# Kernel tuning notes

Measured on AMD Instinct MI355X. Metric: run time of the kernel, lower is better.

Reference implementation:

```python
import jax, jax.numpy as jnp
import numpy as np

N, E, D, H = 50000, 300000, 256, 2
C = D // H  # per-head out_channels (PyG TransformerConv, concat=True)
LN_EPS = 1e-5


def setup_inputs() -> dict:
    key = jax.random.key(0)
    ks = jax.random.split(key, 10)
    s = 1.0 / np.sqrt(D).astype(np.float32)
    return {
        "x": jax.random.normal(ks[0], (N, D), jnp.float32),
        "edge_attr": jax.random.normal(ks[1], (E, D), jnp.float32),
        "edge_index": jax.random.randint(ks[2], (2, E), 0, N, dtype=jnp.int32),
        "Wq": jax.random.normal(ks[3], (D, D), jnp.float32) * s,
        "bq": jnp.zeros((D,), jnp.float32),
        "Wk": jax.random.normal(ks[4], (D, D), jnp.float32) * s,
        "bk": jnp.zeros((D,), jnp.float32),
        "Wv": jax.random.normal(ks[5], (D, D), jnp.float32) * s,
        "bv": jnp.zeros((D,), jnp.float32),
        "We": jax.random.normal(ks[6], (D, D), jnp.float32) * s,  # lin_edge, bias=False in PyG
        "Wskip": jax.random.normal(ks[7], (D, D), jnp.float32) * s,
        "bskip": jnp.zeros((D,), jnp.float32),
        "ln_gamma": jnp.ones((D,), jnp.float32),
        "ln_beta": jnp.zeros((D,), jnp.float32),
    }


def reference(x, edge_attr, edge_index, Wq, bq, Wk, bk, Wv, bv, We,
              Wskip, bskip, ln_gamma, ln_beta):
    src, dst = edge_index[0], edge_index[1]  # message flows src(j) -> dst(i)

    # node-level projections (dense GEMMs), reshaped to [*, H, C]
    q = (x @ Wq + bq).reshape(N, H, C)
    k = (x @ Wk + bk).reshape(N, H, C)
    v = (x @ Wv + bv).reshape(N, H, C)
    e = (edge_attr @ We).reshape(E, H, C)

    # per-edge gather; edge features added to both key and value (PyG TransformerConv)
    k_e = k[src] + e            # [E, H, C]
    v_e = v[src] + e            # [E, H, C]

    # attention logits per edge/head, scaled by sqrt(C)
    alpha = jnp.einsum('ehc,ehc->eh', q[dst], k_e) / np.sqrt(C).astype(np.float32)

    # segment softmax over incoming edges of each destination node
    amax = jax.ops.segment_max(alpha, dst, num_segments=N)   # [N, H]
    ex = jnp.exp(alpha - amax[dst])                          # [E, H]
    denom = jax.ops.segment_sum(ex, dst, num_segments=N)     # [N, H]
    w = ex / (denom[dst] + 1e-16)                            # [E, H]

    # weighted scatter-add aggregation, concat heads
    agg = jax.ops.segment_sum(w[:, :, None] * v_e, dst, num_segments=N)
    out = agg.reshape(N, D)

    # root/skip connection (root_weight=True, beta=False)
    out = out + x @ Wskip + bskip

    # LayerNorm + ReLU
    mu = out.mean(-1, keepdims=True)
    var = out.var(-1, keepdims=True)
    out = (out - mu) * jax.lax.rsqrt(var + LN_EPS) * ln_gamma + ln_beta
    return jax.nn.relu(out)
```

## Files before the change

kernel.cpp:

```cpp
#include <hip/hip_runtime.h>
#include <hip/hip_bf16.h>

#define N_NODES 50000
#define N_EDGES 300000

typedef __attribute__((ext_vector_type(4))) float f32x4;
typedef __attribute__((ext_vector_type(8))) __bf16 bf16x8;
typedef __attribute__((ext_vector_type(4))) __bf16 bf16x4;

__global__ void prep_weights_kernel(const float* __restrict__ Wq, const float* __restrict__ bq,
                                    const float* __restrict__ Wk, const float* __restrict__ bk,
                                    const float* __restrict__ Wv, const float* __restrict__ bv,
                                    const float* __restrict__ Wskip, const float* __restrict__ bskip,
                                    const float* __restrict__ We,
                                    __bf16* __restrict__ Wp, float* __restrict__ bias_p,
                                    __bf16* __restrict__ Wes) {
    int idx = blockIdx.x * 256 + threadIdx.x;
    if (idx < 1024 * 256) {
        int k = idx >> 10, n = idx & 1023;
        int nb = n >> 8, nn = n & 255;
        const float* W = nb == 0 ? Wq : nb == 1 ? Wk : nb == 2 ? Wv : Wskip;
        int step = k >> 5, kg = (k >> 3) & 3, j = k & 7;
        Wp[(((nb * 8 + step) * 1024) + nn * 4 + kg) * 8 + j] = (__bf16)W[k * 256 + nn];
        if (k == 0) {
            const float* b = nb == 0 ? bq : nb == 1 ? bk : nb == 2 ? bv : bskip;
            bias_p[n] = b[nn];
        }
    } else {
        int r = idx - 1024 * 256;
        if (r < 256 * 256) {
            int k = r >> 8, n = r & 255;
            int step = k >> 5, kg = (k >> 3) & 3, j = k & 7;
            Wes[((step * 1024) + n * 4 + kg) * 8 + j] = (__bf16)We[k * 256 + n];
        }
    }
}

__global__ void count_kernel(const int* __restrict__ dst, int* __restrict__ counts) {
    int i = blockIdx.x * 256 + threadIdx.x;
    if (i < N_EDGES) atomicAdd(&counts[dst[i]], 1);
}

__global__ void scan_kernel(const int* __restrict__ counts, int* __restrict__ row_ptr,
                            int* __restrict__ cursor) {
    const int T = 1024;
    const int CPT = (N_NODES + T - 1) / T;
    int tid = threadIdx.x;
    int base = tid * CPT;
    int s = 0;
    for (int j = 0; j < CPT; j++) {
        int idx = base + j;
        if (idx < N_NODES) s += counts[idx];
    }
    __shared__ int buf[T];
    buf[tid] = s;
    __syncthreads();
    for (int off = 1; off < T; off <<= 1) {
        int t = (tid >= off) ? buf[tid - off] : 0;
        __syncthreads();
        buf[tid] += t;
        __syncthreads();
    }
    int run = buf[tid] - s;
    for (int j = 0; j < CPT; j++) {
        int idx = base + j;
        if (idx < N_NODES) {
            row_ptr[idx] = run;
            cursor[idx] = run;
            run += counts[idx];
        }
    }
    if (tid == T - 1) row_ptr[N_NODES] = run;
}

__global__ void scatter_kernel(const int* __restrict__ src, const int* __restrict__ dst,
                               int* __restrict__ cursor, int* __restrict__ cidx,
                               int* __restrict__ sperm) {
    int i = blockIdx.x * 256 + threadIdx.x;
    if (i < N_EDGES) {
        int p = atomicAdd(&cursor[dst[i]], 1);
        cidx[p] = i;
        sperm[p] = src[i];
    }
}

#define BM 128
#define BN 256
#define KD 256

template <typename OutT>
__global__ __launch_bounds__(512, 4) void gemm_kernel(const float* __restrict__ A,
                                                      const int* __restrict__ rowidx, int M,
                                                      const __bf16* __restrict__ Wswz,
                                                      const float* __restrict__ bias, int Nout,
                                                      OutT* __restrict__ C) {
    __shared__ __bf16 As[2][BM * 4 * 8];
    __shared__ __bf16 Bs[2][BN * 4 * 8];
    int tid = threadIdx.x;
    int m0 = blockIdx.x * BM;
    int nb = blockIdx.y;
    int lane = tid & 63, w = tid >> 6;
    int wr = w >> 2, wc = w & 3;
    int l15 = lane & 15, kg4 = lane >> 4;

    f32x4 acc[4][4];
#pragma unroll
    for (int r = 0; r < 4; r++)
#pragma unroll
        for (int c = 0; c < 4; c++) acc[r][c] = (f32x4)0.f;

    int arow = tid >> 2, apart = tid & 3;
    bool aok = (m0 + arow) < M;
    int asrc = aok ? (rowidx ? rowidx[m0 + arow] : (m0 + arow)) : 0;
    const float* Aptr = A + (size_t)asrc * KD + apart * 8;
    const __bf16* Bbase = Wswz + (size_t)nb * 8 * 8192;

    f32x4 a0 = aok ? *reinterpret_cast<const f32x4*>(Aptr) : (f32x4)0.f;
    f32x4 a1 = aok ? *reinterpret_cast<const f32x4*>(Aptr + 4) : (f32x4)0.f;
    bf16x8 b0 = *reinterpret_cast<const bf16x8*>(Bbase + (size_t)tid * 8);
    bf16x8 b1 = *reinterpret_cast<const bf16x8*>(Bbase + (size_t)(tid + 512) * 8);
    {
        bf16x8 ab;
        ab[0] = (__bf16)a0.x; ab[1] = (__bf16)a0.y; ab[2] = (__bf16)a0.z; ab[3] = (__bf16)a0.w;
        ab[4] = (__bf16)a1.x; ab[5] = (__bf16)a1.y; ab[6] = (__bf16)a1.z; ab[7] = (__bf16)a1.w;
        *reinterpret_cast<bf16x8*>(&As[0][tid * 8]) = ab;
        *reinterpret_cast<bf16x8*>(&Bs[0][tid * 8]) = b0;
        *reinterpret_cast<bf16x8*>(&Bs[0][(tid + 512) * 8]) = b1;
    }
    __syncthreads();

    int s = 0;
#pragma unroll
    for (int step = 0; step < 8; ++step) {
        if (step < 7) {
            int k0 = (step + 1) * 32;
            a0 = aok ? *reinterpret_cast<const f32x4*>(Aptr + k0) : (f32x4)0.f;
            a1 = aok ? *reinterpret_cast<const f32x4*>(Aptr + k0 + 4) : (f32x4)0.f;
            b0 = *reinterpret_cast<const bf16x8*>(Bbase + (size_t)((step + 1) * 8192 + tid * 8));
            b1 = *reinterpret_cast<const bf16x8*>(Bbase + (size_t)((step + 1) * 8192 + (tid + 512) * 8));
        }
        bf16x8 af[4], bfr[4];
#pragma unroll
        for (int r = 0; r < 4; r++)
            af[r] = *reinterpret_cast<const bf16x8*>(&As[s][((wr * 64 + r * 16 + l15) * 4 + kg4) * 8]);
#pragma unroll
        for (int c = 0; c < 4; c++)
            bfr[c] = *reinterpret_cast<const bf16x8*>(&Bs[s][((wc * 64 + c * 16 + l15) * 4 + kg4) * 8]);
#pragma unroll
        for (int r = 0; r < 4; r++)
#pragma unroll
            for (int c = 0; c < 4; c++)
                acc[r][c] = __builtin_amdgcn_mfma_f32_16x16x32_bf16(af[r], bfr[c], acc[r][c], 0, 0, 0);
        if (step < 7) {
            bf16x8 ab;
            ab[0] = (__bf16)a0.x; ab[1] = (__bf16)a0.y; ab[2] = (__bf16)a0.z; ab[3] = (__bf16)a0.w;
            ab[4] = (__bf16)a1.x; ab[5] = (__bf16)a1.y; ab[6] = (__bf16)a1.z; ab[7] = (__bf16)a1.w;
            *reinterpret_cast<bf16x8*>(&As[s ^ 1][tid * 8]) = ab;
            *reinterpret_cast<bf16x8*>(&Bs[s ^ 1][tid * 8]) = b0;
            *reinterpret_cast<bf16x8*>(&Bs[s ^ 1][(tid + 512) * 8]) = b1;
        }
        __syncthreads();
        s ^= 1;
    }

#pragma unroll
    for (int r = 0; r < 4; r++) {
        int grow_base = m0 + wr * 64 + r * 16 + kg4 * 4;
#pragma unroll
        for (int i = 0; i < 4; i++) {
            int grow = grow_base + i;
            if (grow < M) {
#pragma unroll
                for (int c = 0; c < 4; c++) {
                    int gcol = nb * BN + wc * 64 + c * 16 + l15;
                    float v = acc[r][c][i];
                    if (bias) v += bias[gcol];
                    C[(size_t)grow * Nout + gcol] = (OutT)v;
                }
            }
        }
    }
}

__global__ __launch_bounds__(256) void attn_kernel(const __bf16* __restrict__ proj,
                                                   const __bf16* __restrict__ eperm,
                                                   const int* __restrict__ sperm,
                                                   const int* __restrict__ row_ptr,
                                                   const float* __restrict__ gamma,
                                                   const float* __restrict__ beta,
                                                   float* __restrict__ out) {
    int w = threadIdx.x >> 6, lane = threadIdx.x & 63;
    int d = blockIdx.x * 4 + w;
    if (d >= N_NODES) return;
    const float rscale = 0.08838834764831845f;

    bf16x4 qb = *reinterpret_cast<const bf16x4*>(proj + (size_t)d * 1024 + lane * 4);
    float q0 = (float)qb.x, q1 = (float)qb.y, q2 = (float)qb.z, q3 = (float)qb.w;
    int start = row_ptr[d], end = row_ptr[d + 1];

    float m = -1e30f, den = 0.f;
    f32x4 acc = (f32x4)0.f;
    int i = start;
    for (; i + 1 < end; i += 2) {
        int s0 = sperm[i], s1 = sperm[i + 1];
        const __bf16* p0 = proj + (size_t)s0 * 1024 + 256 + lane * 4;
        const __bf16* p1 = proj + (size_t)s1 * 1024 + 256 + lane * 4;
        bf16x4 k0 = *reinterpret_cast<const bf16x4*>(p0);
        bf16x4 v0 = *reinterpret_cast<const bf16x4*>(p0 + 256);
        bf16x4 k1 = *reinterpret_cast<const bf16x4*>(p1);
        bf16x4 v1 = *reinterpret_cast<const bf16x4*>(p1 + 256);
        bf16x4 e0 = *reinterpret_cast<const bf16x4*>(eperm + (size_t)i * 256 + lane * 4);
        bf16x4 e1 = *reinterpret_cast<const bf16x4*>(eperm + (size_t)(i + 1) * 256 + lane * 4);
        float e0x = (float)e0.x, e0y = (float)e0.y, e0z = (float)e0.z, e0w = (float)e0.w;
        float e1x = (float)e1.x, e1y = (float)e1.y, e1z = (float)e1.z, e1w = (float)e1.w;
        float pa = q0 * ((float)k0.x + e0x) + q1 * ((float)k0.y + e0y) +
                   q2 * ((float)k0.z + e0z) + q3 * ((float)k0.w + e0w);
        float pb = q0 * ((float)k1.x + e1x) + q1 * ((float)k1.y + e1y) +
                   q2 * ((float)k1.z + e1z) + q3 * ((float)k1.w + e1w);
#pragma unroll
        for (int o = 16; o > 0; o >>= 1) {
            pa += __shfl_xor(pa, o, 32);
            pb += __shfl_xor(pb, o, 32);
        }
        float A0 = pa * rscale, A1 = pb * rscale;
        float mn = fmaxf(m, fmaxf(A0, A1));
        float sc = __expf(m - mn);
        float w0 = __expf(A0 - mn), w1 = __expf(A1 - mn);
        den = den * sc + w0 + w1;
        acc.x = acc.x * sc + w0 * ((float)v0.x + e0x) + w1 * ((float)v1.x + e1x);
        acc.y = acc.y * sc + w0 * ((float)v0.y + e0y) + w1 * ((float)v1.y + e1y);
        acc.z = acc.z * sc + w0 * ((float)v0.z + e0z) + w1 * ((float)v1.z + e1z);
        acc.w = acc.w * sc + w0 * ((float)v0.w + e0w) + w1 * ((float)v1.w + e1w);
        m = mn;
    }
    if (i < end) {
        int s0 = sperm[i];
        const __bf16* p0 = proj + (size_t)s0 * 1024 + 256 + lane * 4;
        bf16x4 k0 = *reinterpret_cast<const bf16x4*>(p0);
        bf16x4 v0 = *reinterpret_cast<const bf16x4*>(p0 + 256);
        bf16x4 e0 = *reinterpret_cast<const bf16x4*>(eperm + (size_t)i * 256 + lane * 4);
        float e0x = (float)e0.x, e0y = (float)e0.y, e0z = (float)e0.z, e0w = (float)e0.w;
        float pa = q0 * ((float)k0.x + e0x) + q1 * ((float)k0.y + e0y) +
                   q2 * ((float)k0.z + e0z) + q3 * ((float)k0.w + e0w);
#pragma unroll
        for (int o = 16; o > 0; o >>= 1) pa += __shfl_xor(pa, o, 32);
        float A0 = pa * rscale;
        float mn = fmaxf(m, A0);
        float sc = __expf(m - mn), w0 = __expf(A0 - mn);
        den = den * sc + w0;
        acc.x = acc.x * sc + w0 * ((float)v0.x + e0x);
        acc.y = acc.y * sc + w0 * ((float)v0.y + e0y);
        acc.z = acc.z * sc + w0 * ((float)v0.z + e0z);
        acc.w = acc.w * sc + w0 * ((float)v0.w + e0w);
    }

    float inv = 1.f / (den + 1e-16f);
    bf16x4 skb = *reinterpret_cast<const bf16x4*>(proj + (size_t)d * 1024 + 768 + lane * 4);
    f32x4 o;
    o.x = acc.x * inv + (float)skb.x;
    o.y = acc.y * inv + (float)skb.y;
    o.z = acc.z * inv + (float)skb.z;
    o.w = acc.w * inv + (float)skb.w;

    float s1 = o.x + o.y + o.z + o.w;
    float s2 = o.x * o.x + o.y * o.y + o.z * o.z + o.w * o.w;
#pragma unroll
    for (int off = 32; off > 0; off >>= 1) {
        s1 += __shfl_xor(s1, off, 64);
        s2 += __shfl_xor(s2, off, 64);
    }
    float mean = s1 * (1.f / 256.f);
    float var = s2 * (1.f / 256.f) - mean * mean;
    float rstd = rsqrtf(var + 1e-5f);
    f32x4 g = *reinterpret_cast<const f32x4*>(gamma + lane * 4);
    f32x4 b = *reinterpret_cast<const f32x4*>(beta + lane * 4);
    o.x = fmaxf(0.f, (o.x - mean) * rstd * g.x + b.x);
    o.y = fmaxf(0.f, (o.y - mean) * rstd * g.y + b.y);
    o.z = fmaxf(0.f, (o.z - mean) * rstd * g.z + b.z);
    o.w = fmaxf(0.f, (o.w - mean) * rstd * g.w + b.w);
    *reinterpret_cast<f32x4*>(out + (size_t)d * 256 + lane * 4) = o;
}

extern "C" void kernel_launch(void* const* d_in, const int* in_sizes, int n_in,
                              void* d_out, int out_size, void* d_ws, size_t ws_size,
                              hipStream_t stream) {
    const float* x = (const float*)d_in[0];
    const float* edge_attr = (const float*)d_in[1];
    const int* edge_index = (const int*)d_in[2];
    const float* Wq = (const float*)d_in[3];
    const float* bq = (const float*)d_in[4];
    const float* Wk = (const float*)d_in[5];
    const float* bk = (const float*)d_in[6];
    const float* Wv = (const float*)d_in[7];
    const float* bv = (const float*)d_in[8];
    const float* We = (const float*)d_in[9];
    const float* Wskip = (const float*)d_in[10];
    const float* bskip = (const float*)d_in[11];
    const float* gamma = (const float*)d_in[12];
    const float* beta = (const float*)d_in[13];
    float* out = (float*)d_out;
    const int* src = edge_index;
    const int* dst = edge_index + N_EDGES;

    char* ws = (char*)d_ws;
    size_t off = 0;
    auto alloc = [&](size_t bytes) {
        size_t p = off;
        off += (bytes + 255) & ~(size_t)255;
        return p;
    };
    __bf16* proj = (__bf16*)(ws + alloc((size_t)N_NODES * 1024 * 2));
    __bf16* eperm = (__bf16*)(ws + alloc((size_t)N_EDGES * 256 * 2));
    __bf16* Wp = (__bf16*)(ws + alloc(1024 * 256 * 2));
    __bf16* Wes = (__bf16*)(ws + alloc(256 * 256 * 2));
    float* bias_p = (float*)(ws + alloc(1024 * 4));
    int* row_ptr = (int*)(ws + alloc((N_NODES + 1) * 4));
    int* cursor = (int*)(ws + alloc(N_NODES * 4));
    int* counts = (int*)(ws + alloc(N_NODES * 4));
    int* cidx = (int*)(ws + alloc(N_EDGES * 4));
    int* sperm = (int*)(ws + alloc(N_EDGES * 4));

    hipMemsetAsync(counts, 0, N_NODES * 4, stream);
    prep_weights_kernel<<<1280, 256, 0, stream>>>(Wq, bq, Wk, bk, Wv, bv, Wskip, bskip, We,
                                                  Wp, bias_p, Wes);
    count_kernel<<<(N_EDGES + 255) / 256, 256, 0, stream>>>(dst, counts);
    scan_kernel<<<1, 1024, 0, stream>>>(counts, row_ptr, cursor);
    scatter_kernel<<<(N_EDGES + 255) / 256, 256, 0, stream>>>(src, dst, cursor, cidx, sperm);
    gemm_kernel<__bf16><<<dim3((N_NODES + BM - 1) / BM, 4), 512, 0, stream>>>(
        x, nullptr, N_NODES, Wp, bias_p, 1024, proj);
    gemm_kernel<__bf16><<<dim3((N_EDGES + BM - 1) / BM, 1), 512, 0, stream>>>(
        edge_attr, cidx, N_EDGES, Wes, nullptr, 256, eperm);
    attn_kernel<<<(N_NODES + 3) / 4, 256, 0, stream>>>(proj, eperm, sperm, row_ptr,
                                                       gamma, beta, out);
}
```

Baseline: 445.6 us.

## Merge GEMM launches, fold memset, stream B via LDS loads, simplify softmax

The node and edge projection GEMMs now run as one launch, with the block index choosing which problem each block handles. Zeroing of the counts buffer moves into the weight-prep kernel. The weight tiles are copied straight into shared memory with global_load_lds, and the scan kernel reads counts as vectors and keeps them in registers. The attention kernel drops the online running-max rescaling in favour of plain exp accumulation, handles four edges per iteration, and folds the 1/sqrt(C) scale into q. The aim is fewer launches and less instruction and latency cost in the gather loop. The price is possible exp overflow if logits grow large, since the max is no longer subtracted.

```diff
diff --git a/kernel.cpp b/kernel.cpp
--- a/kernel.cpp
+++ b/kernel.cpp
@@ -3,19 +3,30 @@
 
 #define N_NODES 50000
 #define N_EDGES 300000
+#define CPAD 53248
 
 typedef __attribute__((ext_vector_type(4))) float f32x4;
+typedef __attribute__((ext_vector_type(4))) int i32x4;
 typedef __attribute__((ext_vector_type(8))) __bf16 bf16x8;
 typedef __attribute__((ext_vector_type(4))) __bf16 bf16x4;
 
-__global__ void prep_weights_kernel(const float* __restrict__ Wq, const float* __restrict__ bq,
-                                    const float* __restrict__ Wk, const float* __restrict__ bk,
-                                    const float* __restrict__ Wv, const float* __restrict__ bv,
-                                    const float* __restrict__ Wskip, const float* __restrict__ bskip,
-                                    const float* __restrict__ We,
-                                    __bf16* __restrict__ Wp, float* __restrict__ bias_p,
-                                    __bf16* __restrict__ Wes) {
-    int idx = blockIdx.x * 256 + threadIdx.x;
+#define GLDS16(g, l)                                                                   \
+    __builtin_amdgcn_global_load_lds((const __attribute__((address_space(1))) void*)(g), \
+                                     (__attribute__((address_space(3))) void*)(l), 16, 0, 0)
+
+__global__ void prep_kernel(const float* __restrict__ Wq, const float* __restrict__ bq,
+                            const float* __restrict__ Wk, const float* __restrict__ bk,
+                            const float* __restrict__ Wv, const float* __restrict__ bv,
+                            const float* __restrict__ Wskip, const float* __restrict__ bskip,
+                            const float* __restrict__ We,
+                            __bf16* __restrict__ Wp, float* __restrict__ bias_p,
+                            __bf16* __restrict__ Wes, int* __restrict__ counts) {
+    int b = blockIdx.x;
+    if (b >= 1280) {
+        counts[(b - 1280) * 256 + threadIdx.x] = 0;
+        return;
+    }
+    int idx = b * 256 + threadIdx.x;
     if (idx < 1024 * 256) {
         int k = idx >> 10, n = idx & 1023;
         int nb = n >> 8, nn = n & 255;
@@ -23,16 +34,14 @@
         int step = k >> 5, kg = (k >> 3) & 3, j = k & 7;
         Wp[(((nb * 8 + step) * 1024) + nn * 4 + kg) * 8 + j] = (__bf16)W[k * 256 + nn];
         if (k == 0) {
-            const float* b = nb == 0 ? bq : nb == 1 ? bk : nb == 2 ? bv : bskip;
-            bias_p[n] = b[nn];
+            const float* bb = nb == 0 ? bq : nb == 1 ? bk : nb == 2 ? bv : bskip;
+            bias_p[n] = bb[nn];
         }
     } else {
         int r = idx - 1024 * 256;
-        if (r < 256 * 256) {
-            int k = r >> 8, n = r & 255;
-            int step = k >> 5, kg = (k >> 3) & 3, j = k & 7;
-            Wes[((step * 1024) + n * 4 + kg) * 8 + j] = (__bf16)We[k * 256 + n];
-        }
+        int k = r >> 8, n = r & 255;
+        int step = k >> 5, kg = (k >> 3) & 3, j = k & 7;
+        Wes[((step * 1024) + n * 4 + kg) * 8 + j] = (__bf16)We[k * 256 + n];
     }
 }
 
@@ -41,36 +50,41 @@
     if (i < N_EDGES) atomicAdd(&counts[dst[i]], 1);
 }
 
-__global__ void scan_kernel(const int* __restrict__ counts, int* __restrict__ row_ptr,
-                            int* __restrict__ cursor) {
-    const int T = 1024;
-    const int CPT = (N_NODES + T - 1) / T;
+__global__ __launch_bounds__(1024) void scan_kernel(const int* __restrict__ counts,
+                                                    int* __restrict__ row_ptr,
+                                                    int* __restrict__ cursor) {
     int tid = threadIdx.x;
-    int base = tid * CPT;
+    int base = tid * 52;
+    int loc[52];
     int s = 0;
-    for (int j = 0; j < CPT; j++) {
-        int idx = base + j;
-        if (idx < N_NODES) s += counts[idx];
-    }
-    __shared__ int buf[T];
+#pragma unroll
+    for (int j = 0; j < 13; j++) {
+        i32x4 v = *reinterpret_cast<const i32x4*>(counts + base + j * 4);
+        loc[j * 4 + 0] = v.x; loc[j * 4 + 1] = v.y;
+        loc[j * 4 + 2] = v.z; loc[j * 4 + 3] = v.w;
+        s += v.x + v.y + v.z + v.w;
+    }
+    __shared__ int buf[1024];
     buf[tid] = s;
     __syncthreads();
-    for (int off = 1; off < T; off <<= 1) {
+    for (int off = 1; off < 1024; off <<= 1) {
         int t = (tid >= off) ? buf[tid - off] : 0;
         __syncthreads();
         buf[tid] += t;
         __syncthreads();
     }
     int run = buf[tid] - s;
-    for (int j = 0; j < CPT; j++) {
+#pragma unroll
+    for (int j = 0; j < 52; j++) {
         int idx = base + j;
         if (idx < N_NODES) {
             row_ptr[idx] = run;
             cursor[idx] = run;
-            run += counts[idx];
-        }
-    }
-    if (tid == T - 1) row_ptr[N_NODES] = run;
+            run += loc[j];
+        } else if (idx == N_NODES) {
+            row_ptr[N_NODES] = run;
+        }
+    }
 }
 
 __global__ void scatter_kernel(const int* __restrict__ src, const int* __restrict__ dst,
@@ -84,21 +98,30 @@
     }
 }
 
-#define BM 128
-#define BN 256
-#define KD 256
-
-template <typename OutT>
-__global__ __launch_bounds__(512, 4) void gemm_kernel(const float* __restrict__ A,
-                                                      const int* __restrict__ rowidx, int M,
-                                                      const __bf16* __restrict__ Wswz,
-                                                      const float* __restrict__ bias, int Nout,
-                                                      OutT* __restrict__ C) {
-    __shared__ __bf16 As[2][BM * 4 * 8];
-    __shared__ __bf16 Bs[2][BN * 4 * 8];
+__global__ __launch_bounds__(512, 4) void gemm_kernel(
+    const float* __restrict__ xA, const __bf16* __restrict__ Wp,
+    const float* __restrict__ bias_p, __bf16* __restrict__ proj,
+    const float* __restrict__ eA, const int* __restrict__ cidx,
+    const __bf16* __restrict__ Wes, __bf16* __restrict__ eperm, int nodeBlocks) {
+    __shared__ __bf16 As[2][128 * 32];
+    __shared__ __bf16 Bs[2][256 * 32];
     int tid = threadIdx.x;
-    int m0 = blockIdx.x * BM;
-    int nb = blockIdx.y;
+
+    const float* A; const int* rowidx; int M, Nout, m0, nb;
+    const __bf16* Wsw; const float* bias; __bf16* C;
+    if ((int)blockIdx.x < nodeBlocks) {
+        int t = blockIdx.x;
+        nb = t & 3; m0 = (t >> 2) * 128;
+        A = xA; rowidx = nullptr; M = N_NODES; Nout = 1024;
+        Wsw = Wp; bias = bias_p; C = proj;
+    } else {
+        int t = blockIdx.x - nodeBlocks;
+        nb = 0; m0 = t * 128;
+        A = eA; rowidx = cidx; M = N_EDGES; Nout = 256;
+        Wsw = Wes; bias = nullptr; C = eperm;
+    }
+    const __bf16* Bbase = Wsw + (size_t)nb * 65536;
+
     int lane = tid & 63, w = tid >> 6;
     int wr = w >> 2, wc = w & 3;
     int l15 = lane & 15, kg4 = lane >> 4;
@@ -111,21 +134,19 @@
 
     int arow = tid >> 2, apart = tid & 3;
     bool aok = (m0 + arow) < M;
-    int asrc = aok ? (rowidx ? rowidx[m0 + arow] : (m0 + arow)) : 0;
-    const float* Aptr = A + (size_t)asrc * KD + apart * 8;
-    const __bf16* Bbase = Wswz + (size_t)nb * 8 * 8192;
+    int asrc = 0;
+    if (aok) asrc = rowidx ? rowidx[m0 + arow] : (m0 + arow);
+    const float* Aptr = A + (size_t)asrc * 256 + apart * 8;
 
     f32x4 a0 = aok ? *reinterpret_cast<const f32x4*>(Aptr) : (f32x4)0.f;
     f32x4 a1 = aok ? *reinterpret_cast<const f32x4*>(Aptr + 4) : (f32x4)0.f;
-    bf16x8 b0 = *reinterpret_cast<const bf16x8*>(Bbase + (size_t)tid * 8);
-    bf16x8 b1 = *reinterpret_cast<const bf16x8*>(Bbase + (size_t)(tid + 512) * 8);
+    GLDS16(Bbase + (size_t)tid * 8, &Bs[0][w * 64 * 8]);
+    GLDS16(Bbase + (size_t)(tid + 512) * 8, &Bs[0][(512 + w * 64) * 8]);
     {
         bf16x8 ab;
         ab[0] = (__bf16)a0.x; ab[1] = (__bf16)a0.y; ab[2] = (__bf16)a0.z; ab[3] = (__bf16)a0.w;
         ab[4] = (__bf16)a1.x; ab[5] = (__bf16)a1.y; ab[6] = (__bf16)a1.z; ab[7] = (__bf16)a1.w;
         *reinterpret_cast<bf16x8*>(&As[0][tid * 8]) = ab;
-        *reinterpret_cast<bf16x8*>(&Bs[0][tid * 8]) = b0;
-        *reinterpret_cast<bf16x8*>(&Bs[0][(tid + 512) * 8]) = b1;
     }
     __syncthreads();
 
@@ -136,8 +157,9 @@
             int k0 = (step + 1) * 32;
             a0 = aok ? *reinterpret_cast<const f32x4*>(Aptr + k0) : (f32x4)0.f;
             a1 = aok ? *reinterpret_cast<const f32x4*>(Aptr + k0 + 4) : (f32x4)0.f;
-            b0 = *reinterpret_cast<const bf16x8*>(Bbase + (size_t)((step + 1) * 8192 + tid * 8));
-            b1 = *reinterpret_cast<const bf16x8*>(Bbase + (size_t)((step + 1) * 8192 + (tid + 512) * 8));
+            GLDS16(Bbase + (size_t)((step + 1) * 8192 + tid * 8), &Bs[s ^ 1][w * 64 * 8]);
+            GLDS16(Bbase + (size_t)((step + 1) * 8192 + (tid + 512) * 8),
+                   &Bs[s ^ 1][(512 + w * 64) * 8]);
         }
         bf16x8 af[4], bfr[4];
 #pragma unroll
@@ -156,8 +178,6 @@
             ab[0] = (__bf16)a0.x; ab[1] = (__bf16)a0.y; ab[2] = (__bf16)a0.z; ab[3] = (__bf16)a0.w;
             ab[4] = (__bf16)a1.x; ab[5] = (__bf16)a1.y; ab[6] = (__bf16)a1.z; ab[7] = (__bf16)a1.w;
             *reinterpret_cast<bf16x8*>(&As[s ^ 1][tid * 8]) = ab;
-            *reinterpret_cast<bf16x8*>(&Bs[s ^ 1][tid * 8]) = b0;
-            *reinterpret_cast<bf16x8*>(&Bs[s ^ 1][(tid + 512) * 8]) = b1;
         }
         __syncthreads();
         s ^= 1;
@@ -165,17 +185,17 @@
 
 #pragma unroll
     for (int r = 0; r < 4; r++) {
-        int grow_base = m0 + wr * 64 + r * 16 + kg4 * 4;
-#pragma unroll
-        for (int i = 0; i < 4; i++) {
-            int grow = grow_base + i;
+        int growb = m0 + wr * 64 + r * 16 + kg4 * 4;
+#pragma unroll
+        for (int i2 = 0; i2 < 4; i2++) {
+            int grow = growb + i2;
             if (grow < M) {
 #pragma unroll
                 for (int c = 0; c < 4; c++) {
-                    int gcol = nb * BN + wc * 64 + c * 16 + l15;
-                    float v = acc[r][c][i];
-                    if (bias) v += bias[gcol];
-                    C[(size_t)grow * Nout + gcol] = (OutT)v;
+                    int lcol = wc * 64 + c * 16 + l15;
+                    float v = acc[r][c][i2];
+                    if (bias) v += bias[nb * 256 + lcol];
+                    C[(size_t)grow * Nout + nb * 256 + lcol] = (__bf16)v;
                 }
             }
         }
@@ -195,63 +215,62 @@
     const float rscale = 0.08838834764831845f;
 
     bf16x4 qb = *reinterpret_cast<const bf16x4*>(proj + (size_t)d * 1024 + lane * 4);
-    float q0 = (float)qb.x, q1 = (float)qb.y, q2 = (float)qb.z, q3 = (float)qb.w;
+    float q0 = (float)qb.x * rscale, q1 = (float)qb.y * rscale;
+    float q2 = (float)qb.z * rscale, q3 = (float)qb.w * rscale;
     int start = row_ptr[d], end = row_ptr[d + 1];
 
-    float m = -1e30f, den = 0.f;
+    float den = 0.f;
     f32x4 acc = (f32x4)0.f;
     int i = start;
-    for (; i + 1 < end; i += 2) {
-        int s0 = sperm[i], s1 = sperm[i + 1];
-        const __bf16* p0 = proj + (size_t)s0 * 1024 + 256 + lane * 4;
-        const __bf16* p1 = proj + (size_t)s1 * 1024 + 256 + lane * 4;
-        bf16x4 k0 = *reinterpret_cast<const bf16x4*>(p0);
-        bf16x4 v0 = *reinterpret_cast<const bf16x4*>(p0 + 256);
-        bf16x4 k1 = *reinterpret_cast<const bf16x4*>(p1);
-        bf16x4 v1 = *reinterpret_cast<const bf16x4*>(p1 + 256);
+    int n4 = start + ((end - start) & ~3);
+    for (; i < n4; i += 4) {
+        int sA[4];
+#pragma unroll
+        for (int j = 0; j < 4; j++) sA[j] = sperm[i + j];
+        bf16x4 kA[4], vA[4], eE[4];
+#pragma unroll
+        for (int j = 0; j < 4; j++) {
+            const __bf16* pr = proj + (size_t)sA[j] * 1024 + 256 + lane * 4;
+            kA[j] = *reinterpret_cast<const bf16x4*>(pr);
+            vA[j] = *reinterpret_cast<const bf16x4*>(pr + 256);
+            eE[j] = *reinterpret_cast<const bf16x4*>(eperm + (size_t)(i + j) * 256 + lane * 4);
+        }
+        float p[4];
+#pragma unroll
+        for (int j = 0; j < 4; j++)
+            p[j] = q0 * ((float)kA[j].x + (float)eE[j].x) + q1 * ((float)kA[j].y + (float)eE[j].y) +
+                   q2 * ((float)kA[j].z + (float)eE[j].z) + q3 * ((float)kA[j].w + (float)eE[j].w);
+#pragma unroll
+        for (int o = 16; o > 0; o >>= 1) {
+#pragma unroll
+            for (int j = 0; j < 4; j++) p[j] += __shfl_xor(p[j], o, 32);
+        }
+#pragma unroll
+        for (int j = 0; j < 4; j++) {
+            float wj = __expf(p[j]);
+            den += wj;
+            acc.x += wj * ((float)vA[j].x + (float)eE[j].x);
+            acc.y += wj * ((float)vA[j].y + (float)eE[j].y);
+            acc.z += wj * ((float)vA[j].z + (float)eE[j].z);
+            acc.w += wj * ((float)vA[j].w + (float)eE[j].w);
+        }
+    }
+    for (; i < end; ++i) {
+        int s0 = sperm[i];
+        const __bf16* pr = proj + (size_t)s0 * 1024 + 256 + lane * 4;
+        bf16x4 k0 = *reinterpret_cast<const bf16x4*>(pr);
+        bf16x4 v0 = *reinterpret_cast<const bf16x4*>(pr + 256);
         bf16x4 e0 = *reinterpret_cast<const bf16x4*>(eperm + (size_t)i * 256 + lane * 4);
-        bf16x4 e1 = *reinterpret_cast<const bf16x4*>(eperm + (size_t)(i + 1) * 256 + lane * 4);
-        float e0x = (float)e0.x, e0y = (float)e0.y, e0z = (float)e0.z, e0w = (float)e0.w;
-        float e1x = (float)e1.x, e1y = (float)e1.y, e1z = (float)e1.z, e1w = (float)e1.w;
-        float pa = q0 * ((float)k0.x + e0x) + q1 * ((float)k0.y + e0y) +
-                   q2 * ((float)k0.z + e0z) + q3 * ((float)k0.w + e0w);
-        float pb = q0 * ((float)k1.x + e1x) + q1 * ((float)k1.y + e1y) +
-                   q2 * ((float)k1.z + e1z) + q3 * ((float)k1.w + e1w);
-#pragma unroll
-        for (int o = 16; o > 0; o >>= 1) {
-            pa += __shfl_xor(pa, o, 32);
-            pb += __shfl_xor(pb, o, 32);
-        }
-        float A0 = pa * rscale, A1 = pb * rscale;
-        float mn = fmaxf(m, fmaxf(A0, A1));
-        float sc = __expf(m - mn);
-        float w0 = __expf(A0 - mn), w1 = __expf(A1 - mn);
-        den = den * sc + w0 + w1;
-        acc.x = acc.x * sc + w0 * ((float)v0.x + e0x) + w1 * ((float)v1.x + e1x);
-        acc.y = acc.y * sc + w0 * ((float)v0.y + e0y) + w1 * ((float)v1.y + e1y);
-        acc.z = acc.z * sc + w0 * ((float)v0.z + e0z) + w1 * ((float)v1.z + e1z);
-        acc.w = acc.w * sc + w0 * ((float)v0.w + e0w) + w1 * ((float)v1.w + e1w);
-        m = mn;
-    }
-    if (i < end) {
-        int s0 = sperm[i];
-        const __bf16* p0 = proj + (size_t)s0 * 1024 + 256 + lane * 4;
-        bf16x4 k0 = *reinterpret_cast<const bf16x4*>(p0);
-        bf16x4 v0 = *reinterpret_cast<const bf16x4*>(p0 + 256);
-        bf16x4 e0 = *reinterpret_cast<const bf16x4*>(eperm + (size_t)i * 256 + lane * 4);
-        float e0x = (float)e0.x, e0y = (float)e0.y, e0z = (float)e0.z, e0w = (float)e0.w;
-        float pa = q0 * ((float)k0.x + e0x) + q1 * ((float)k0.y + e0y) +
-                   q2 * ((float)k0.z + e0z) + q3 * ((float)k0.w + e0w);
-#pragma unroll
-        for (int o = 16; o > 0; o >>= 1) pa += __shfl_xor(pa, o, 32);
-        float A0 = pa * rscale;
-        float mn = fmaxf(m, A0);
-        float sc = __expf(m - mn), w0 = __expf(A0 - mn);
-        den = den * sc + w0;
-        acc.x = acc.x * sc + w0 * ((float)v0.x + e0x);
-        acc.y = acc.y * sc + w0 * ((float)v0.y + e0y);
-        acc.z = acc.z * sc + w0 * ((float)v0.z + e0z);
-        acc.w = acc.w * sc + w0 * ((float)v0.w + e0w);
+        float p = q0 * ((float)k0.x + (float)e0.x) + q1 * ((float)k0.y + (float)e0.y) +
+                  q2 * ((float)k0.z + (float)e0.z) + q3 * ((float)k0.w + (float)e0.w);
+#pragma unroll
+        for (int o = 16; o > 0; o >>= 1) p += __shfl_xor(p, o, 32);
+        float wj = __expf(p);
+        den += wj;
+        acc.x += wj * ((float)v0.x + (float)e0.x);
+        acc.y += wj * ((float)v0.y + (float)e0.y);
+        acc.z += wj * ((float)v0.z + (float)e0.z);
+        acc.w += wj * ((float)v0.w + (float)e0.w);
     }
 
     float inv = 1.f / (den + 1e-16f);
@@ -316,20 +335,20 @@
     float* bias_p = (float*)(ws + alloc(1024 * 4));
     int* row_ptr = (int*)(ws + alloc((N_NODES + 1) * 4));
     int* cursor = (int*)(ws + alloc(N_NODES * 4));
-    int* counts = (int*)(ws + alloc(N_NODES * 4));
+    int* counts = (int*)(ws + alloc(CPAD * 4));
     int* cidx = (int*)(ws + alloc(N_EDGES * 4));
     int* sperm = (int*)(ws + alloc(N_EDGES * 4));
 
-    hipMemsetAsync(counts, 0, N_NODES * 4, stream);
-    prep_weights_kernel<<<1280, 256, 0, stream>>>(Wq, bq, Wk, bk, Wv, bv, Wskip, bskip, We,
-                                                  Wp, bias_p, Wes);
+    int nodeBlocks = ((N_NODES + 127) / 128) * 4;
+    int edgeBlocks = (N_EDGES + 127) / 128;
+
+    prep_kernel<<<1488, 256, 0, stream>>>(Wq, bq, Wk, bk, Wv, bv, Wskip, bskip, We,
+                                          Wp, bias_p, Wes, counts);
     count_kernel<<<(N_EDGES + 255) / 256, 256, 0, stream>>>(dst, counts);
     scan_kernel<<<1, 1024, 0, stream>>>(counts, row_ptr, cursor);
     scatter_kernel<<<(N_EDGES + 255) / 256, 256, 0, stream>>>(src, dst, cursor, cidx, sperm);
-    gemm_kernel<__bf16><<<dim3((N_NODES + BM - 1) / BM, 4), 512, 0, stream>>>(
-        x, nullptr, N_NODES, Wp, bias_p, 1024, proj);
-    gemm_kernel<__bf16><<<dim3((N_EDGES + BM - 1) / BM, 1), 512, 0, stream>>>(
-        edge_attr, cidx, N_EDGES, Wes, nullptr, 256, eperm);
+    gemm_kernel<<<nodeBlocks + edgeBlocks, 512, 0, stream>>>(
+        x, Wp, bias_p, proj, edge_attr, cidx, Wes, eperm, nodeBlocks);
     attn_kernel<<<(N_NODES + 3) / 4, 256, 0, stream>>>(proj, eperm, sperm, row_ptr,
                                                        gamma, beta, out);
 }
```

Result: faster. 372.4 us (-16.4%).
